# Kernel optimization log

Measured on AMD Instinct MI355X. Metric: run time of the kernel, lower is better.

The kernel has to match this reference:

```python
import jax, jax.numpy as jnp
import numpy as np

HIDDEN_DIM = 128


def setup_inputs() -> dict:
    key = jax.random.key(0)
    ks = jax.random.split(key, 7)
    n_edges, edge_dim, edge_hidden, d = 20000, 16, 128, HIDDEN_DIM
    h_v = jax.random.normal(ks[0], (n_edges, d), dtype=jnp.float32)
    h_w = jax.random.normal(ks[1], (n_edges, d), dtype=jnp.float32)
    edge_features = jax.random.normal(ks[2], (n_edges, edge_dim), dtype=jnp.float32)
    W1 = jax.random.normal(ks[3], (edge_dim, edge_hidden), dtype=jnp.float32) * (1.0 / np.sqrt(edge_dim))
    b1 = jnp.zeros((edge_hidden,), dtype=jnp.float32)
    W2 = jax.random.normal(ks[4], (edge_hidden, d * d), dtype=jnp.float32) * (1.0 / np.sqrt(edge_hidden))
    b2 = jnp.zeros((d * d,), dtype=jnp.float32)
    return {"h_v": h_v, "h_w": h_w, "edge_features": edge_features,
            "W1": W1, "b1": b1, "W2": W2, "b2": b2}


def reference(h_v, h_w, edge_features, W1, b1, W2, b2):
    d = HIDDEN_DIM
    # Edge MLP: edge_dim -> edge_hidden -> d*d
    hidden = jax.nn.relu(edge_features @ W1 + b1)          # (E, edge_hidden)
    A = (hidden @ W2 + b2).reshape(-1, d, d)               # (E, d, d) per-edge matrices
    # Batched matrix-vector product: messages_e = A_e @ h_w_e
    messages = jnp.einsum('eij,ej->ei', A, h_w)            # (E, d)
    return messages
```

## Files before the change

kernel.cpp:

```cpp
#include <hip/hip_runtime.h>

#define E_EDGES 20000
#define D_DIM   128
#define SLAB_DW 5376

#define NBA 132
#define NBH 313
#define NBC 320
#define NBD 250

typedef __bf16 bf16x8 __attribute__((ext_vector_type(8)));
typedef float  floatx4 __attribute__((ext_vector_type(4)));

__device__ __forceinline__ unsigned short f32_to_bf16_rne(float f) {
    unsigned int u = __float_as_uint(f);
    unsigned int r = u + 0x7FFFu + ((u >> 16) & 1u);
    return (unsigned short)(r >> 16);
}

__device__ __forceinline__ void gload_lds16(const void* g, void* l) {
    __builtin_amdgcn_global_load_lds(
        (const __attribute__((address_space(1))) unsigned int*)g,
        (__attribute__((address_space(3))) unsigned int*)l, 16, 0, 0);
}

__global__ __launch_bounds__(256) void prep_all(
    const float* __restrict__ W2, const float* __restrict__ b2,
    const float* __restrict__ ef, const float* __restrict__ W1,
    const float* __restrict__ b1, const float* __restrict__ hw,
    uint4* __restrict__ bpf, unsigned int* __restrict__ hTp2,
    unsigned short* __restrict__ hwb, float* __restrict__ outz)
{
    __shared__ __align__(16) char pmem[34816];
    const int bx = blockIdx.x;
    const int t  = threadIdx.x;

    if (bx < NBA) {
        const int h = bx;
        if (h < 129) {
            unsigned short* tile = (unsigned short*)pmem;
            const float* src = (h < 128) ? (W2 + (size_t)h * (D_DIM * D_DIM)) : b2;
            #pragma unroll
            for (int r = 0; r < 16; ++r) {
                const float4 v = ((const float4*)src)[r * 256 + t];
                int c   = (r * 256 + t) * 4;
                int col = c >> 7;
                int k   = c & 127;
                unsigned int u0 = f32_to_bf16_rne(v.x) | ((unsigned int)f32_to_bf16_rne(v.y) << 16);
                unsigned int u1 = f32_to_bf16_rne(v.z) | ((unsigned int)f32_to_bf16_rne(v.w) << 16);
                *(uint2*)&tile[col * 136 + k] = make_uint2(u0, u1);
            }
            __syncthreads();
            #pragma unroll
            for (int r2 = 0; r2 < 8; ++r2) {
                int cidx = r2 * 256 + t;
                int ll = cidx & 63;
                int sp = (cidx >> 6) & 1;
                int gp = (cidx >> 7) & 3;
                int ks = (cidx >> 9) & 1;
                int ch = (cidx >> 10) & 1;
                int col = 64 * ch + 16 * gp + (ll & 15);
                int k0  = 64 * ks + 32 * sp + 8 * (ll >> 4);
                bpf[(size_t)h * 2048 + cidx] = *(const uint4*)&tile[col * 136 + k0];
            }
        } else {
            #pragma unroll
            for (int r2 = 0; r2 < 8; ++r2)
                bpf[(size_t)h * 2048 + r2 * 256 + t] = make_uint4(0, 0, 0, 0);
        }
    } else if (bx < NBA + NBH) {
        float (*lds_ef)[17] = (float(*)[17])pmem;
        const int b  = bx - NBA;
        const int e0 = b * 64;
        {
            int e  = t >> 2;
            int k4 = (t & 3) * 4;
            int ge = e0 + e;
            float4 v = make_float4(0.f, 0.f, 0.f, 0.f);
            if (ge < E_EDGES) v = *(const float4*)(ef + (size_t)ge * 16 + k4);
            lds_ef[e][k4 + 0] = v.x; lds_ef[e][k4 + 1] = v.y;
            lds_ef[e][k4 + 2] = v.z; lds_ef[e][k4 + 3] = v.w;
        }
        __syncthreads();
        const int e  = t & 63;
        const int hg = t >> 6;
        const int ge = e0 + e;
        const bool valid = ge < E_EDGES;
        const int eg = ge / 80;
        const int re = ge - eg * 80;
        unsigned int* slab = hTp2 + (size_t)eg * SLAB_DW;
        float efr[16];
        #pragma unroll
        for (int k = 0; k < 16; ++k) efr[k] = lds_ef[e][k];
        #pragma unroll 4
        for (int hi2 = 0; hi2 < 16; ++hi2) {
            const int h0 = __builtin_amdgcn_readfirstlane(hg * 32 + 2 * hi2);
            float a0 = b1[h0], a1 = b1[h0 + 1];
            #pragma unroll
            for (int k = 0; k < 16; ++k) {
                a0 += efr[k] * W1[k * 128 + h0];
                a1 += efr[k] * W1[k * 128 + h0 + 1];
            }
            unsigned int pk = (unsigned int)f32_to_bf16_rne(fmaxf(a0, 0.f))
                            | ((unsigned int)f32_to_bf16_rne(fmaxf(a1, 0.f)) << 16);
            if (valid) slab[(hg * 16 + hi2) * 80 + re] = pk;
        }
        if (hg == 0 && valid) {
            slab[64 * 80 + re] = 0x00003F80u;
            slab[65 * 80 + re] = 0u;
        }
    } else if (bx < NBA + NBH + NBC) {
        int i0 = (bx - NBA - NBH) * 256 + t;
        for (int i = i0; i < (E_EDGES * D_DIM) / 4; i += NBC * 256) {
            const float4 v = ((const float4*)hw)[i];
            union { unsigned short u16[4]; uint2 u2; } o;
            o.u16[0] = f32_to_bf16_rne(v.x);
            o.u16[1] = f32_to_bf16_rne(v.y);
            o.u16[2] = f32_to_bf16_rne(v.z);
            o.u16[3] = f32_to_bf16_rne(v.w);
            ((uint2*)hwb)[i] = o.u2;
        }
    } else {
        int i0 = (bx - NBA - NBH - NBC) * 256 + t;
        float4* o4 = (float4*)outz;
        for (int i = i0; i < (E_EDGES * D_DIM) / 4; i += NBD * 256)
            o4[i] = make_float4(0.f, 0.f, 0.f, 0.f);
    }
}

__global__ __launch_bounds__(256, 4)
void edge_main(const uint4* __restrict__ bpf, const unsigned int* __restrict__ hTp2,
               const uint4* __restrict__ hwb, float* __restrict__ out) {
    __shared__ __align__(16) char slab[21504];
    const int bx  = blockIdx.x;
    const int eg  = bx >> 2;
    const int ch  = (bx >> 1) & 1;
    const int ks  = bx & 1;
    const int tid = threadIdx.x;
    const int w   = tid >> 6;
    const int l   = tid & 63;
    const int l4  = l >> 4;
    const int lm  = l & 15;
    const int e0  = eg * 80;

    {
        const char* src = (const char*)(hTp2 + (size_t)eg * SLAB_DW);
        for (int i = w; i < 21; i += 4)
            gload_lds16(src + i * 1024 + l * 16, slab + i * 1024);
    }

    bf16x8 A[5][2];
    #pragma unroll
    for (int m = 0; m < 5; ++m)
        #pragma unroll
        for (int sp = 0; sp < 2; ++sp)
            A[m][sp] = ((const bf16x8*)hwb)[(e0 + 16 * m + lm) * 16 + 8 * ks + 4 * sp + l4];

    floatx4 C[5];
    #pragma unroll
    for (int m = 0; m < 5; ++m) C[m] = (floatx4){0.f, 0.f, 0.f, 0.f};
    const floatx4 Zf = (floatx4){0.f, 0.f, 0.f, 0.f};

    __syncthreads();

    const bf16x8* bpf8 = (const bf16x8*)bpf;
    const int cbase = ch * 1024 + ks * 512 + w * 128 + l;

    bf16x8 Ba[2], Bb[2];
    auto loadB = [&](int h, bf16x8 (&B)[2]) {
        const bf16x8* p = bpf8 + (size_t)h * 2048 + cbase;
        B[0] = p[0];
        B[1] = p[64];
    };
    auto computeH = [&](const bf16x8 (&B)[2], const uint4 (&hp)[5], bool odd) {
        #pragma unroll
        for (int m = 0; m < 5; ++m) {
            floatx4 D = __builtin_amdgcn_mfma_f32_16x16x32_bf16(A[m][0], B[0], Zf, 0, 0, 0);
            D = __builtin_amdgcn_mfma_f32_16x16x32_bf16(A[m][1], B[1], D, 0, 0, 0);
            #pragma unroll
            for (int r = 0; r < 4; ++r) {
                unsigned int u = hp[m][r];
                float sc = odd ? __uint_as_float(u & 0xFFFF0000u)
                               : __uint_as_float(u << 16);
                C[m][r] += sc * D[r];
            }
        }
    };

    loadB(0, Ba);
    for (int q = 0; q < 65; ++q) {
        uint4 hp[5];
        #pragma unroll
        for (int m = 0; m < 5; ++m)
            hp[m] = *(const uint4*)(slab + q * 320 + m * 64 + l4 * 16);
        loadB(2 * q + 1, Bb);
        computeH(Ba, hp, false);
        loadB(2 * q + 2, Ba);
        computeH(Bb, hp, true);
    }

    #pragma unroll
    for (int m = 0; m < 5; ++m)
        #pragma unroll
        for (int r = 0; r < 4; ++r)
            atomicAdd(&out[(size_t)(e0 + 16 * m + 4 * l4 + r) * D_DIM
                           + 64 * ch + 16 * w + lm], C[m][r]);
}

extern "C" void kernel_launch(void* const* d_in, const int* in_sizes, int n_in,
                              void* d_out, int out_size, void* d_ws, size_t ws_size,
                              hipStream_t stream) {
    const float* h_w = (const float*)d_in[1];
    const float* ef  = (const float*)d_in[2];
    const float* W1  = (const float*)d_in[3];
    const float* b1  = (const float*)d_in[4];
    const float* W2  = (const float*)d_in[5];
    const float* b2  = (const float*)d_in[6];
    float* out = (float*)d_out;

    char* ws = (char*)d_ws;
    uint4*          bpf  = (uint4*)ws;
    unsigned int*   hTp2 = (unsigned int*)(ws + 4325376);
    unsigned short* hwb  = (unsigned short*)(ws + 4325376 + 5397504);

    hipLaunchKernelGGL(prep_all, dim3(NBA + NBH + NBC + NBD), dim3(256), 0, stream,
                       W2, b2, ef, W1, b1, h_w, bpf, hTp2, hwb, out);
    hipLaunchKernelGGL(edge_main, dim3(1000), dim3(256), 0, stream,
                       bpf, hTp2, (const uint4*)hwb, out);
}
```

Before: 187.6 us.

## Scale h_w by hidden in f16 before MFMA, accumulating directly into C

The old loop ran the MFMA into a fresh product for each hidden unit and then did a scalar multiply-accumulate into C. The new loop first multiplies h_w by the hidden activation with packed f16 operations, then feeds the scaled operand straight into MFMAs that accumulate into C. This drops the per-hidden VALU scale-and-add on the fp32 outputs, at the cost of packed f16 multiplies on the inputs. To support this, the hidden slab is re-laid out per edge (row stride 264 bytes), everything moves from bf16 to f16, and the prep kernel now stages W1 and b1 in LDS. f16 has a narrower range and the products are rounded to f16 before the MFMA, so accuracy may change.

```diff
diff --git a/kernel.cpp b/kernel.cpp
--- a/kernel.cpp
+++ b/kernel.cpp
@@ -2,20 +2,24 @@
 
 #define E_EDGES 20000
 #define D_DIM   128
-#define SLAB_DW 5376
 
 #define NBA 132
 #define NBH 313
 #define NBC 320
 #define NBD 250
 
-typedef __bf16 bf16x8 __attribute__((ext_vector_type(8)));
-typedef float  floatx4 __attribute__((ext_vector_type(4)));
-
-__device__ __forceinline__ unsigned short f32_to_bf16_rne(float f) {
-    unsigned int u = __float_as_uint(f);
-    unsigned int r = u + 0x7FFFu + ((u >> 16) & 1u);
-    return (unsigned short)(r >> 16);
+#define SLAB_B  21504
+#define BPF_SL  136
+
+typedef _Float16 f16x8 __attribute__((ext_vector_type(8)));
+typedef _Float16 f16x2 __attribute__((ext_vector_type(2)));
+typedef float    floatx4 __attribute__((ext_vector_type(4)));
+
+union F8 { f16x8 v; f16x2 h2[4]; unsigned int u[4]; };
+
+__device__ __forceinline__ unsigned short f32_to_f16(float f) {
+    _Float16 h = (_Float16)f;
+    return __builtin_bit_cast(unsigned short, h);
 }
 
 __device__ __forceinline__ void gload_lds16(const void* g, void* l) {
@@ -28,7 +32,7 @@
     const float* __restrict__ W2, const float* __restrict__ b2,
     const float* __restrict__ ef, const float* __restrict__ W1,
     const float* __restrict__ b1, const float* __restrict__ hw,
-    uint4* __restrict__ bpf, unsigned int* __restrict__ hTp2,
+    uint4* __restrict__ bpf, char* __restrict__ hslab,
     unsigned short* __restrict__ hwb, float* __restrict__ outz)
 {
     __shared__ __align__(16) char pmem[34816];
@@ -46,8 +50,8 @@
                 int c   = (r * 256 + t) * 4;
                 int col = c >> 7;
                 int k   = c & 127;
-                unsigned int u0 = f32_to_bf16_rne(v.x) | ((unsigned int)f32_to_bf16_rne(v.y) << 16);
-                unsigned int u1 = f32_to_bf16_rne(v.z) | ((unsigned int)f32_to_bf16_rne(v.w) << 16);
+                unsigned int u0 = f32_to_f16(v.x) | ((unsigned int)f32_to_f16(v.y) << 16);
+                unsigned int u1 = f32_to_f16(v.z) | ((unsigned int)f32_to_f16(v.w) << 16);
                 *(uint2*)&tile[col * 136 + k] = make_uint2(u0, u1);
             }
             __syncthreads();
@@ -69,17 +73,23 @@
                 bpf[(size_t)h * 2048 + r2 * 256 + t] = make_uint4(0, 0, 0, 0);
         }
     } else if (bx < NBA + NBH) {
-        float (*lds_ef)[17] = (float(*)[17])pmem;
+        float* W1s = (float*)pmem;
+        float* b1s = (float*)(pmem + 8192);
+        float (*efs)[17] = (float(*)[17])(pmem + 8704);
         const int b  = bx - NBA;
         const int e0 = b * 64;
+        #pragma unroll
+        for (int i = 0; i < 2; ++i)
+            *(float4*)&W1s[(i * 256 + t) * 4] = ((const float4*)W1)[i * 256 + t];
+        if (t < 32) *(float4*)&b1s[t * 4] = ((const float4*)b1)[t];
         {
             int e  = t >> 2;
             int k4 = (t & 3) * 4;
             int ge = e0 + e;
             float4 v = make_float4(0.f, 0.f, 0.f, 0.f);
             if (ge < E_EDGES) v = *(const float4*)(ef + (size_t)ge * 16 + k4);
-            lds_ef[e][k4 + 0] = v.x; lds_ef[e][k4 + 1] = v.y;
-            lds_ef[e][k4 + 2] = v.z; lds_ef[e][k4 + 3] = v.w;
+            efs[e][k4 + 0] = v.x; efs[e][k4 + 1] = v.y;
+            efs[e][k4 + 2] = v.z; efs[e][k4 + 3] = v.w;
         }
         __syncthreads();
         const int e  = t & 63;
@@ -88,36 +98,38 @@
         const bool valid = ge < E_EDGES;
         const int eg = ge / 80;
         const int re = ge - eg * 80;
-        unsigned int* slab = hTp2 + (size_t)eg * SLAB_DW;
+        char* slab = hslab + (size_t)eg * SLAB_B + re * 264;
         float efr[16];
         #pragma unroll
-        for (int k = 0; k < 16; ++k) efr[k] = lds_ef[e][k];
+        for (int k = 0; k < 16; ++k) efr[k] = efs[e][k];
         #pragma unroll 4
         for (int hi2 = 0; hi2 < 16; ++hi2) {
-            const int h0 = __builtin_amdgcn_readfirstlane(hg * 32 + 2 * hi2);
-            float a0 = b1[h0], a1 = b1[h0 + 1];
+            const int h0 = hg * 32 + 2 * hi2;
+            float2 bb = *(const float2*)&b1s[h0];
+            float a0 = bb.x, a1 = bb.y;
             #pragma unroll
             for (int k = 0; k < 16; ++k) {
-                a0 += efr[k] * W1[k * 128 + h0];
-                a1 += efr[k] * W1[k * 128 + h0 + 1];
-            }
-            unsigned int pk = (unsigned int)f32_to_bf16_rne(fmaxf(a0, 0.f))
-                            | ((unsigned int)f32_to_bf16_rne(fmaxf(a1, 0.f)) << 16);
-            if (valid) slab[(hg * 16 + hi2) * 80 + re] = pk;
+                float2 wv = *(const float2*)&W1s[k * 128 + h0];
+                a0 += efr[k] * wv.x;
+                a1 += efr[k] * wv.y;
+            }
+            unsigned int pk = (unsigned int)f32_to_f16(fmaxf(a0, 0.f))
+                            | ((unsigned int)f32_to_f16(fmaxf(a1, 0.f)) << 16);
+            if (valid) *(unsigned int*)(slab + h0 * 2) = pk;
         }
         if (hg == 0 && valid) {
-            slab[64 * 80 + re] = 0x00003F80u;
-            slab[65 * 80 + re] = 0u;
+            *(unsigned int*)(slab + 128 * 2) = 0x00003C00u;
+            *(unsigned int*)(slab + 130 * 2) = 0u;
         }
     } else if (bx < NBA + NBH + NBC) {
         int i0 = (bx - NBA - NBH) * 256 + t;
         for (int i = i0; i < (E_EDGES * D_DIM) / 4; i += NBC * 256) {
             const float4 v = ((const float4*)hw)[i];
             union { unsigned short u16[4]; uint2 u2; } o;
-            o.u16[0] = f32_to_bf16_rne(v.x);
-            o.u16[1] = f32_to_bf16_rne(v.y);
-            o.u16[2] = f32_to_bf16_rne(v.z);
-            o.u16[3] = f32_to_bf16_rne(v.w);
+            o.u16[0] = f32_to_f16(v.x);
+            o.u16[1] = f32_to_f16(v.y);
+            o.u16[2] = f32_to_f16(v.z);
+            o.u16[3] = f32_to_f16(v.w);
             ((uint2*)hwb)[i] = o.u2;
         }
     } else {
@@ -129,9 +141,9 @@
 }
 
 __global__ __launch_bounds__(256, 4)
-void edge_main(const uint4* __restrict__ bpf, const unsigned int* __restrict__ hTp2,
+void edge_main(const uint4* __restrict__ bpf, const char* __restrict__ hslab,
                const uint4* __restrict__ hwb, float* __restrict__ out) {
-    __shared__ __align__(16) char slab[21504];
+    __shared__ __align__(16) char slab[SLAB_B];
     const int bx  = blockIdx.x;
     const int eg  = bx >> 2;
     const int ch  = (bx >> 1) & 1;
@@ -144,60 +156,76 @@
     const int e0  = eg * 80;
 
     {
-        const char* src = (const char*)(hTp2 + (size_t)eg * SLAB_DW);
+        const char* src = hslab + (size_t)eg * SLAB_B;
         for (int i = w; i < 21; i += 4)
             gload_lds16(src + i * 1024 + l * 16, slab + i * 1024);
     }
 
-    bf16x8 A[5][2];
+    F8 hwh[5][2];
     #pragma unroll
     for (int m = 0; m < 5; ++m)
         #pragma unroll
-        for (int sp = 0; sp < 2; ++sp)
-            A[m][sp] = ((const bf16x8*)hwb)[(e0 + 16 * m + lm) * 16 + 8 * ks + 4 * sp + l4];
+        for (int jq = 0; jq < 2; ++jq)
+            hwh[m][jq].v = ((const F8*)hwb)[(e0 + 16 * m + lm) * 16 + 8 * ks + 4 * jq + l4].v;
 
     floatx4 C[5];
     #pragma unroll
     for (int m = 0; m < 5; ++m) C[m] = (floatx4){0.f, 0.f, 0.f, 0.f};
-    const floatx4 Zf = (floatx4){0.f, 0.f, 0.f, 0.f};
 
     __syncthreads();
 
-    const bf16x8* bpf8 = (const bf16x8*)bpf;
+    const f16x8* bpf8 = (const f16x8*)bpf;
     const int cbase = ch * 1024 + ks * 512 + w * 128 + l;
 
-    bf16x8 Ba[2], Bb[2];
-    auto loadB = [&](int h, bf16x8 (&B)[2]) {
-        const bf16x8* p = bpf8 + (size_t)h * 2048 + cbase;
+    f16x8 Bbuf[2][2];
+    auto loadB = [&](int h, f16x8 (&B)[2]) {
+        const f16x8* p = bpf8 + (size_t)h * 2048 + cbase;
         B[0] = p[0];
         B[1] = p[64];
     };
-    auto computeH = [&](const bf16x8 (&B)[2], const uint4 (&hp)[5], bool odd) {
-        #pragma unroll
-        for (int m = 0; m < 5; ++m) {
-            floatx4 D = __builtin_amdgcn_mfma_f32_16x16x32_bf16(A[m][0], B[0], Zf, 0, 0, 0);
-            D = __builtin_amdgcn_mfma_f32_16x16x32_bf16(A[m][1], B[1], D, 0, 0, 0);
-            #pragma unroll
-            for (int r = 0; r < 4; ++r) {
-                unsigned int u = hp[m][r];
-                float sc = odd ? __uint_as_float(u & 0xFFFF0000u)
-                               : __uint_as_float(u << 16);
-                C[m][r] += sc * D[r];
-            }
-        }
+    auto loadHid = [&](int h4, uint2 (&hid)[5]) {
+        #pragma unroll
+        for (int m = 0; m < 5; ++m)
+            hid[m] = *(const uint2*)(slab + (16 * m + lm) * 264 + h4 * 8);
     };
-
-    loadB(0, Ba);
-    for (int q = 0; q < 65; ++q) {
-        uint4 hp[5];
-        #pragma unroll
-        for (int m = 0; m < 5; ++m)
-            hp[m] = *(const uint4*)(slab + q * 320 + m * 64 + l4 * 16);
-        loadB(2 * q + 1, Bb);
-        computeH(Ba, hp, false);
-        loadB(2 * q + 2, Ba);
-        computeH(Bb, hp, true);
+    auto group4 = [&](int h4, const uint2 (&hid)[5]) {
+        #pragma unroll
+        for (int hh = 0; hh < 4; ++hh) {
+            const int h = 4 * h4 + hh;
+            const int p = h & 1;
+            f16x2 d[5];
+            #pragma unroll
+            for (int m = 0; m < 5; ++m) {
+                unsigned int s   = (hh < 2) ? hid[m].x : hid[m].y;
+                unsigned int sel = (hh & 1) ? 0x03020302u : 0x01000100u;
+                d[m] = __builtin_bit_cast(f16x2, __builtin_amdgcn_perm(0u, s, sel));
+            }
+            #pragma unroll
+            for (int m = 0; m < 5; ++m) {
+                F8 a0, a1;
+                #pragma unroll
+                for (int i = 0; i < 4; ++i) {
+                    a0.h2[i] = hwh[m][0].h2[i] * d[m];
+                    a1.h2[i] = hwh[m][1].h2[i] * d[m];
+                }
+                C[m] = __builtin_amdgcn_mfma_f32_16x16x32_f16(a0.v, Bbuf[p][0], C[m], 0, 0, 0);
+                C[m] = __builtin_amdgcn_mfma_f32_16x16x32_f16(a1.v, Bbuf[p][1], C[m], 0, 0, 0);
+            }
+            loadB(h + 2, Bbuf[p]);
+        }
+    };
+
+    loadB(0, Bbuf[0]);
+    loadB(1, Bbuf[1]);
+    uint2 hidA[5], hidB[5];
+    loadHid(0, hidA);
+    for (int h4 = 0; h4 < 32; h4 += 2) {
+        loadHid(h4 + 1, hidB);
+        group4(h4, hidA);
+        loadHid(h4 + 2, hidA);
+        group4(h4 + 1, hidB);
     }
+    group4(32, hidA);
 
     #pragma unroll
     for (int m = 0; m < 5; ++m)
@@ -219,12 +247,12 @@
     float* out = (float*)d_out;
 
     char* ws = (char*)d_ws;
-    uint4*          bpf  = (uint4*)ws;
-    unsigned int*   hTp2 = (unsigned int*)(ws + 4325376);
-    unsigned short* hwb  = (unsigned short*)(ws + 4325376 + 5397504);
+    uint4*          bpf   = (uint4*)ws;
+    char*           hslab = ws + 4456448;
+    unsigned short* hwb   = (unsigned short*)(ws + 4456448 + 5376000);
 
     hipLaunchKernelGGL(prep_all, dim3(NBA + NBH + NBC + NBD), dim3(256), 0, stream,
-                       W2, b2, ef, W1, b1, h_w, bpf, hTp2, hwb, out);
+                       W2, b2, ef, W1, b1, h_w, bpf, hslab, hwb, out);
     hipLaunchKernelGGL(edge_main, dim3(1000), dim3(256), 0, stream,
-                       bpf, hTp2, (const uint4*)hwb, out);
-}
+                       bpf, hslab, (const uint4*)hwb, out);
+}
```

Result: faster. 180.5 us (-3.8%).
